# Optimization experiments

Hardware: AMD Instinct MI355X
Metric: run time of the kernel (lower is better)

Reference implementation:

```python
import jax, jax.numpy as jnp
import numpy as np

EMBED_DIM = 1024
NUM_HEADS = 16
HEAD_DIM = EMBED_DIM // NUM_HEADS
SEQ_LEN = 2048
BATCH = 2


def setup_inputs() -> dict:
    key = jax.random.key(0)
    ks = jax.random.split(key, 9)
    s = 1.0 / np.sqrt(EMBED_DIM)
    inputs = jax.random.normal(ks[0], (BATCH, SEQ_LEN, EMBED_DIM), dtype=jnp.float32)
    Wq = jax.random.uniform(ks[1], (EMBED_DIM, EMBED_DIM), jnp.float32, -s, s)
    bq = jax.random.uniform(ks[2], (EMBED_DIM,), jnp.float32, -s, s)
    Wk = jax.random.uniform(ks[3], (EMBED_DIM, EMBED_DIM), jnp.float32, -s, s)
    bk = jax.random.uniform(ks[4], (EMBED_DIM,), jnp.float32, -s, s)
    Wv = jax.random.uniform(ks[5], (EMBED_DIM, EMBED_DIM), jnp.float32, -s, s)
    bv = jax.random.uniform(ks[6], (EMBED_DIM,), jnp.float32, -s, s)
    Wo = jax.random.uniform(ks[7], (EMBED_DIM, EMBED_DIM), jnp.float32, -s, s)
    bo = jax.random.uniform(ks[8], (EMBED_DIM,), jnp.float32, -s, s)
    return {"inputs": inputs, "Wq": Wq, "bq": bq, "Wk": Wk, "bk": bk,
            "Wv": Wv, "bv": bv, "Wo": Wo, "bo": bo}


def reference(inputs, Wq, bq, Wk, bk, Wv, bv, Wo, bo):
    B, S, D = inputs.shape
    H, Hd = NUM_HEADS, HEAD_DIM

    def heads(x):  # [B,S,D] -> [B,H,S,Hd]
        return x.reshape(B, S, H, Hd).transpose(0, 2, 1, 3)

    q = heads(inputs @ Wq + bq)
    k = heads(inputs @ Wk + bk)
    v = heads(inputs @ Wv + bv)

    # [B,H,S,S] causal scores (naive, matching original module)
    scores = jnp.einsum('bhqd,bhkd->bhqk', q, k) * (Hd ** -0.5)
    causal = jnp.tril(jnp.ones((S, S), dtype=bool))
    scores = jnp.where(causal, scores, jnp.float32(-jnp.inf))
    attn = jax.nn.softmax(scores, axis=-1)

    out = jnp.einsum('bhqk,bhkd->bhqd', attn, v)
    out = out.transpose(0, 2, 1, 3).reshape(B, S, D)
    return out @ Wo + bo
```

## Files before the change

kernel.cpp:

```cpp
#include <hip/hip_runtime.h>
#include <stdint.h>
#include <stddef.h>

#define SEQ   2048
#define DIM   1024
#define NH    16
#define HD    64
#define MTOT  4096
#define LPAD  72
#define EPAD  136
#define FPAD  132

typedef __attribute__((ext_vector_type(8))) short short8;
typedef __attribute__((ext_vector_type(4))) float floatx4;
typedef __attribute__((ext_vector_type(16))) float floatx16;
typedef __attribute__((ext_vector_type(4))) float float4v;
typedef __attribute__((ext_vector_type(4))) unsigned short ushort4v;
typedef __attribute__((ext_vector_type(4))) unsigned int uint4v;

__device__ __forceinline__ floatx4 mfma_bf16(short8 a, short8 b, floatx4 c) {
    return __builtin_amdgcn_mfma_f32_16x16x32_bf16(a, b, c, 0, 0, 0);
}
__device__ __forceinline__ floatx16 mfma32(short8 a, short8 b, floatx16 c) {
    return __builtin_amdgcn_mfma_f32_32x32x16_bf16(a, b, c, 0, 0, 0);
}

__device__ __forceinline__ float b2f(unsigned short s) {
    unsigned int u = ((unsigned int)s) << 16;
    return __builtin_bit_cast(float, u);
}
__device__ __forceinline__ unsigned short f2b(float f) {
    unsigned int u = __builtin_bit_cast(unsigned int, f);
    u += 0x7fffu + ((u >> 16) & 1u);
    return (unsigned short)(u >> 16);
}
__device__ __forceinline__ unsigned int cvtpk(float lo, float hi) {
    unsigned int w;
    asm("v_cvt_pk_bf16_f32 %0, %1, %2" : "=v"(w) : "v"(lo), "v"(hi));
    return w;
}
__device__ __forceinline__ void swap32(unsigned int& a, unsigned int& b) {
    asm("v_permlane32_swap_b32 %0, %1" : "+v"(a), "+v"(b));
}
__device__ __forceinline__ short8 mk8(unsigned int a, unsigned int b,
                                      unsigned int c, unsigned int d) {
    uint4v u; u.x = a; u.y = b; u.z = c; u.w = d;
    return __builtin_bit_cast(short8, u);
}
__device__ __forceinline__ void g2l16(const unsigned short* g, unsigned short* l) {
    __builtin_amdgcn_global_load_lds(
        (const __attribute__((address_space(1))) void*)g,
        (__attribute__((address_space(3))) void*)l, 16, 0, 0);
}

__global__ __launch_bounds__(256) void cvt_f32_bf16(const float* __restrict__ in,
                                                    unsigned short* __restrict__ out) {
    const int i = (blockIdx.x * 256 + threadIdx.x) * 4;
    const float4v v = *(const float4v*)&in[i];
    ushort4v o;
    o.x = f2b(v.x); o.y = f2b(v.y); o.z = f2b(v.z); o.w = f2b(v.w);
    *(ushort4v*)&out[i] = o;
}

__global__ __launch_bounds__(256) void transpose_all(const float* __restrict__ w0,
                                                     const float* __restrict__ w1,
                                                     const float* __restrict__ w2,
                                                     const float* __restrict__ w3,
                                                     unsigned short* __restrict__ outbase) {
    __shared__ float t[64][65];
    const int z = blockIdx.z;
    const float* in = (z == 0) ? w0 : (z == 1) ? w1 : (z == 2) ? w2 : w3;
    unsigned short* out = outbase + (size_t)z * DIM * DIM;
    const int c0 = blockIdx.x * 64, r0 = blockIdx.y * 64;
    const int x = threadIdx.x, y = threadIdx.y;
#pragma unroll
    for (int i = 0; i < 64; i += 4)
        t[y + i][x] = in[(size_t)(r0 + y + i) * DIM + c0 + x];
    __syncthreads();
#pragma unroll
    for (int i = 0; i < 64; i += 4)
        out[(size_t)(c0 + y + i) * DIM + r0 + x] = f2b(t[x][y + i]);
}

__global__ __launch_bounds__(256) void gemm_fused(const unsigned short* __restrict__ A,
                                                  const unsigned short* __restrict__ WTbase,
                                                  const float* __restrict__ b0,
                                                  const float* __restrict__ b1,
                                                  const float* __restrict__ b2,
                                                  void* __restrict__ outbase,
                                                  int qkv) {
    __shared__ __attribute__((aligned(16))) unsigned short smem[2 * 128 * LPAD];
    unsigned short* As = smem;
    unsigned short* Bs = smem + 128 * 64;

    const int z = blockIdx.z;
    const unsigned short* BT = WTbase + (size_t)z * (DIM * DIM);
    const float* bias        = (z == 0) ? b0 : (z == 1) ? b1 : b2;
    const int mode = qkv ? ((z == 0) ? 1 : (z == 1) ? 3 : 4) : 0;
    float* Cf          = (float*)outbase;
    unsigned short* Cb = (unsigned short*)outbase + (size_t)z * ((size_t)MTOT * DIM);

    const int tid = threadIdx.x;
    const int w = tid >> 6, lane = tid & 63;
    const int quad = lane >> 4, l16 = lane & 15;
    const int wm = w >> 1, wn = w & 1;
    const int m0 = blockIdx.x * 128, n0 = blockIdx.y * 128;
    const int bb = m0 >> 11;

    floatx4 acc[4][4];
#pragma unroll
    for (int mi = 0; mi < 4; ++mi)
#pragma unroll
        for (int ni = 0; ni < 4; ++ni) acc[mi][ni] = (floatx4)0.0f;

    const int srow8 = lane >> 3;
    const int sgs8  = ((lane & 7) ^ srow8) * 8;
    const unsigned short* gA = &A [(size_t)(m0 + w * 8 + srow8) * DIM + sgs8];
    const unsigned short* gB = &BT[(size_t)(n0 + w * 8 + srow8) * DIM + sgs8];

    const int sx = l16 & 7;

    for (int k0 = 0; ; k0 += 64) {
#pragma unroll
        for (int i = 0; i < 4; ++i) {
            g2l16(gA + (size_t)i * (32 * DIM) + k0, &As[(i * 4 + w) * 512]);
            g2l16(gB + (size_t)i * (32 * DIM) + k0, &Bs[(i * 4 + w) * 512]);
        }
        __syncthreads();
#pragma unroll
        for (int kk = 0; kk < 2; ++kk) {
            short8 a[4], b[4];
#pragma unroll
            for (int mi = 0; mi < 4; ++mi)
                a[mi] = *(const short8*)&As[(wm * 64 + mi * 16 + l16) * 64 +
                                            (((kk * 4) + quad) ^ sx) * 8];
#pragma unroll
            for (int ni = 0; ni < 4; ++ni)
                b[ni] = *(const short8*)&Bs[(wn * 64 + ni * 16 + l16) * 64 +
                                            (((kk * 4) + quad) ^ sx) * 8];
#pragma unroll
            for (int mi = 0; mi < 4; ++mi)
#pragma unroll
                for (int ni = 0; ni < 4; ++ni)
                    acc[mi][ni] = mfma_bf16(a[mi], b[ni], acc[mi][ni]);
        }
        if (k0 + 64 >= DIM) break;
        __syncthreads();
    }

    float bvv[4];
#pragma unroll
    for (int ni = 0; ni < 4; ++ni) bvv[ni] = bias[n0 + wn * 64 + ni * 16 + l16];

    if (mode == 0) {
        float* T = (float*)smem;
        for (int p = 0; p < 4; ++p) {
            __syncthreads();
            if (wm == (p >> 1)) {
                const int mib = (p & 1) * 2;
#pragma unroll
                for (int mm = 0; mm < 2; ++mm)
#pragma unroll
                    for (int ni = 0; ni < 4; ++ni)
#pragma unroll
                        for (int r = 0; r < 4; ++r)
                            T[(mm * 16 + quad * 4 + r) * FPAD + wn * 64 + ni * 16 + l16] =
                                acc[mib + mm][ni][r] + bvv[ni];
            }
            __syncthreads();
#pragma unroll
            for (int it = 0; it < 4; ++it) {
                const int c = it * 256 + tid;
                const int row = c >> 5, nof = (c & 31) * 4;
                *(float4v*)&Cf[(size_t)(m0 + p * 32 + row) * DIM + n0 + nof] =
                    *(const float4v*)&T[row * FPAD + nof];
            }
        }
    } else if (mode == 1) {
        unsigned short* T = smem;
        __syncthreads();
#pragma unroll
        for (int mi = 0; mi < 4; ++mi)
#pragma unroll
            for (int ni = 0; ni < 4; ++ni)
#pragma unroll
                for (int r = 0; r < 4; ++r)
                    T[(wm * 64 + mi * 16 + quad * 4 + r) * EPAD + wn * 64 + ni * 16 + l16] =
                        f2b(acc[mi][ni][r] + bvv[ni]);
        __syncthreads();
#pragma unroll
        for (int it = 0; it < 8; ++it) {
            const int c = it * 256 + tid;
            const int seg = c >> 3, d8 = (c & 7) * 8;
            const int mm = seg >> 1, hseg = seg & 1;
            const int h = (n0 >> 6) + hseg;
            const int s = (m0 & (SEQ - 1)) + mm;
            *(short8*)&Cb[((size_t)(bb * NH + h) * SEQ + s) * HD + d8] =
                *(const short8*)&T[mm * EPAD + hseg * 64 + d8];
        }
    } else if (mode == 3) {
        unsigned short* T = smem;
        __syncthreads();
#pragma unroll
        for (int mi = 0; mi < 4; ++mi)
#pragma unroll
            for (int ni = 0; ni < 4; ++ni)
#pragma unroll
                for (int r = 0; r < 4; ++r)
                    T[(wm * 64 + mi * 16 + quad * 4 + r) * EPAD + wn * 64 + ni * 16 + l16] =
                        f2b(acc[mi][ni][r] + bvv[ni]);
        __syncthreads();
#pragma unroll
        for (int it = 0; it < 8; ++it) {
            const int f = it * 256 + tid;
            const int ln = f & 63, fragid = f >> 6;
            const int h2 = fragid >> 4;
            const int jb = (fragid >> 2) & 3;
            const int c  = fragid & 3;
            const short8 v = *(const short8*)&T[(jb * 32 + (ln & 31)) * EPAD +
                                                h2 * 64 + c * 16 + (ln >> 5) * 8];
            const int bh = bb * NH + (n0 >> 6) + h2;
            const int jg = ((m0 & (SEQ - 1)) >> 5) + jb;
            *(short8*)&Cb[(((size_t)bh * 64 + jg) * 4 + c) * 512 + ln * 8] = v;
        }
    } else {
        unsigned short* T = smem;
        __syncthreads();
#pragma unroll
        for (int mi = 0; mi < 4; ++mi)
#pragma unroll
            for (int ni = 0; ni < 4; ++ni) {
                ushort4v pk;
#pragma unroll
                for (int r = 0; r < 4; ++r) pk[r] = f2b(acc[mi][ni][r] + bvv[ni]);
                *(ushort4v*)&T[(wn * 64 + ni * 16 + l16) * EPAD + wm * 64 + mi * 16 + quad * 4] = pk;
            }
        __syncthreads();
#pragma unroll
        for (int it = 0; it < 8; ++it) {
            const int f = it * 256 + tid;
            const int ln = f & 63, fragid = f >> 6;
            const int h2 = fragid >> 4;
            const int jb = (fragid >> 2) & 3;
            const int dk = fragid & 3;
            const int d0 = dk >> 1, kk = dk & 1;
            const short8 v = *(const short8*)&T[(h2 * 64 + d0 * 32 + (ln & 31)) * EPAD +
                                                jb * 32 + kk * 16 + (ln >> 5) * 8];
            const int bh = bb * NH + (n0 >> 6) + h2;
            const int jg = ((m0 & (SEQ - 1)) >> 5) + jb;
            *(short8*)&Cb[(((size_t)bh * 64 + jg) * 4 + dk) * 512 + ln * 8] = v;
        }
    }
}

__global__ __launch_bounds__(64) void attn_fwd(const unsigned short* __restrict__ Q,
                                               const unsigned short* __restrict__ KP,
                                               const unsigned short* __restrict__ VP,
                                               unsigned short* __restrict__ O) {
    __shared__ __attribute__((aligned(16))) unsigned short Os[32 * LPAD];
    __shared__ float Linv[32];

    const int bh = blockIdx.x;
    const int qc = (gridDim.y - 1) - blockIdx.y;
    const int lane = threadIdx.x;
    const int ql  = lane & 31;
    const int hi  = lane >> 5;
    const int hi4 = hi * 4;
    const int hi8 = hi * 8;

    const unsigned short* Qh  = Q  + (size_t)bh * SEQ * HD;
    const unsigned short* KPh = KP + (size_t)bh * (64 * 2048);
    const unsigned short* VPh = VP + (size_t)bh * (64 * 2048);
    const int q0 = qc * 32;

    short8 qf[4];
#pragma unroll
    for (int c = 0; c < 4; ++c) {
        short8 t = *(const short8*)(Qh + (size_t)(q0 + ql) * HD + c * 16 + hi8);
        short8 o;
#pragma unroll
        for (int e = 0; e < 8; ++e)
            o[e] = (short)f2b(b2f((unsigned short)t[e]) * 0.125f);
        qf[c] = o;
    }

    floatx16 o_acc0 = (floatx16)0.0f, o_acc1 = (floatx16)0.0f;
    float l0 = 0.0f, l1 = 0.0f;

#define LOADKV(KF, VF, JJ) do {                                              \
        const unsigned short* kb_ = KPh + (size_t)(JJ) * 2048 + lane * 8;    \
        const unsigned short* vb_ = VPh + (size_t)(JJ) * 2048 + lane * 8;    \
        _Pragma("unroll")                                                    \
        for (int c_ = 0; c_ < 4; ++c_) {                                     \
            KF[c_] = *(const short8*)(kb_ + c_ * 512);                       \
            VF[c_] = *(const short8*)(vb_ + c_ * 512);                       \
        }                                                                    \
    } while (0)

#define ATT_BLOCK(KF, VF, MASKED) do {                                       \
        floatx16 st_ = (floatx16)0.0f;                                       \
        _Pragma("unroll")                                                    \
        for (int c_ = 0; c_ < 4; ++c_) st_ = mfma32(KF[c_], qf[c_], st_);    \
        float p_[16];                                                        \
        _Pragma("unroll")                                                    \
        for (int r_ = 0; r_ < 16; ++r_) {                                    \
            float e_ = __expf(st_[r_]);                                      \
            if (MASKED)                                                      \
                e_ = (((r_ & 3) + 8 * (r_ >> 2) + hi4) > ql) ? 0.0f : e_;    \
            p_[r_] = e_;                                                     \
        }                                                                    \
        l0 += (p_[0] + p_[1]) + (p_[2] + p_[3]);                             \
        l1 += (p_[4] + p_[5]) + (p_[6] + p_[7]);                             \
        l0 += (p_[8] + p_[9]) + (p_[10] + p_[11]);                           \
        l1 += (p_[12] + p_[13]) + (p_[14] + p_[15]);                         \
        unsigned int w0_ = cvtpk(p_[0], p_[1]),   w2_ = cvtpk(p_[4], p_[5]); \
        unsigned int w1_ = cvtpk(p_[2], p_[3]),   w3_ = cvtpk(p_[6], p_[7]); \
        unsigned int w4_ = cvtpk(p_[8], p_[9]),   w6_ = cvtpk(p_[12], p_[13]); \
        unsigned int w5_ = cvtpk(p_[10], p_[11]), w7_ = cvtpk(p_[14], p_[15]); \
        swap32(w0_, w2_); swap32(w1_, w3_);                                  \
        swap32(w4_, w6_); swap32(w5_, w7_);                                  \
        const short8 pa0_ = mk8(w0_, w1_, w2_, w3_);                         \
        const short8 pa1_ = mk8(w4_, w5_, w6_, w7_);                         \
        o_acc0 = mfma32(pa0_, VF[0], o_acc0);                                \
        o_acc0 = mfma32(pa1_, VF[1], o_acc0);                                \
        o_acc1 = mfma32(pa0_, VF[2], o_acc1);                                \
        o_acc1 = mfma32(pa1_, VF[3], o_acc1);                                \
    } while (0)

    short8 kfA[4], vfA[4], kfB[4], vfB[4];
    LOADKV(kfA, vfA, 0);
    int j = 0;
    while (j + 2 <= qc) {
        LOADKV(kfB, vfB, j + 1);
        ATT_BLOCK(kfA, vfA, 0);
        LOADKV(kfA, vfA, j + 2);
        ATT_BLOCK(kfB, vfB, 0);
        j += 2;
    }
    if (j < qc) {
        LOADKV(kfB, vfB, qc);
        ATT_BLOCK(kfA, vfA, 0);
        ATT_BLOCK(kfB, vfB, 1);
    } else {
        ATT_BLOCK(kfA, vfA, 1);
    }

    float l = l0 + l1;
    l += __shfl_xor(l, 32, 64);
    const float inv = 1.0f / l;
    if (lane < 32) Linv[lane] = inv;
    __syncthreads();
#pragma unroll
    for (int r = 0; r < 16; ++r) {
        const int row = (r & 3) + 8 * (r >> 2) + hi4;
        const float iv = Linv[row];
        Os[row * LPAD + ql]      = f2b(o_acc0[r] * iv);
        Os[row * LPAD + 32 + ql] = f2b(o_acc1[r] * iv);
    }
    __syncthreads();
    const int bb = bh >> 4, h = bh & 15;
#pragma unroll
    for (int it = 0; it < 4; ++it) {
        const int row = it * 8 + (lane >> 3), d8 = (lane & 7) * 8;
        *(short8*)&O[(size_t)(bb * SEQ + q0 + row) * DIM + h * HD + d8] =
            *(const short8*)&Os[row * LPAD + d8];
    }
#undef LOADKV
#undef ATT_BLOCK
}

extern "C" void kernel_launch(void* const* d_in, const int* in_sizes, int n_in,
                              void* d_out, int out_size, void* d_ws, size_t ws_size,
                              hipStream_t stream) {
    const float* X  = (const float*)d_in[0];
    const float* Wq = (const float*)d_in[1];
    const float* bq = (const float*)d_in[2];
    const float* Wk = (const float*)d_in[3];
    const float* bk = (const float*)d_in[4];
    const float* Wv = (const float*)d_in[5];
    const float* bv = (const float*)d_in[6];
    const float* Wo = (const float*)d_in[7];
    const float* bo = (const float*)d_in[8];

    unsigned short* ws = (unsigned short*)d_ws;
    const size_t WSZ = (size_t)DIM * DIM;
    const size_t TSZ = (size_t)MTOT * DIM;
    unsigned short* WqT = ws;
    unsigned short* WoT = ws + 3 * WSZ;
    unsigned short* Qb  = ws + 4 * WSZ;
    unsigned short* Kp  = Qb + TSZ;
    unsigned short* Vp  = Kp + TSZ;
    unsigned short* Ob  = Vp + TSZ;

    unsigned short* Xb = (unsigned short*)d_out;

    cvt_f32_bf16<<<dim3(TSZ / 1024), 256, 0, stream>>>(X, Xb);

    transpose_all<<<dim3(16, 16, 4), dim3(64, 4), 0, stream>>>(Wq, Wk, Wv, Wo, WqT);

    gemm_fused<<<dim3(MTOT / 128, DIM / 128, 3), 256, 0, stream>>>(
        Xb, WqT, bq, bk, bv, (void*)Qb, 1);

    attn_fwd<<<dim3(2 * NH, SEQ / 32), 64, 0, stream>>>(Qb, Kp, Vp, Ob);

    gemm_fused<<<dim3(MTOT / 128, DIM / 128, 1), 256, 0, stream>>>(
        Ob, WoT, bo, bo, bo, d_out, 0);
}
```

Before: 171.2 us.

## Split attention KV loop across four waves per block with LDS reduction

Each attention block now runs four waves, each handling every fourth KV block for the same 32 query rows. Their unnormalized outputs and row sums are combined through shared memory before normalizing and writing out. This cuts the serial KV chain per block, which is long for late query chunks, and adds MFMA priority hints. In exchange it uses more LDS and adds a cross-wave reduction, and waves on early query chunks sit idle.

```diff
diff --git a/kernel.cpp b/kernel.cpp
--- a/kernel.cpp
+++ b/kernel.cpp
@@ -253,16 +253,17 @@
     }
 }
 
-__global__ __launch_bounds__(64) void attn_fwd(const unsigned short* __restrict__ Q,
-                                               const unsigned short* __restrict__ KP,
-                                               const unsigned short* __restrict__ VP,
-                                               unsigned short* __restrict__ O) {
-    __shared__ __attribute__((aligned(16))) unsigned short Os[32 * LPAD];
-    __shared__ float Linv[32];
+__global__ __launch_bounds__(256) void attn_fwd(const unsigned short* __restrict__ Q,
+                                                const unsigned short* __restrict__ KP,
+                                                const unsigned short* __restrict__ VP,
+                                                unsigned short* __restrict__ O) {
+    __shared__ float Fo[4][32][68];
+    __shared__ float Fl[4][32];
 
     const int bh = blockIdx.x;
     const int qc = (gridDim.y - 1) - blockIdx.y;
-    const int lane = threadIdx.x;
+    const int tid = threadIdx.x;
+    const int w = tid >> 6, lane = tid & 63;
     const int ql  = lane & 31;
     const int hi  = lane >> 5;
     const int hi4 = hi * 4;
@@ -299,8 +300,10 @@
 
 #define ATT_BLOCK(KF, VF, MASKED) do {                                       \
         floatx16 st_ = (floatx16)0.0f;                                       \
+        __builtin_amdgcn_s_setprio(1);                                       \
         _Pragma("unroll")                                                    \
         for (int c_ = 0; c_ < 4; ++c_) st_ = mfma32(KF[c_], qf[c_], st_);    \
+        __builtin_amdgcn_s_setprio(0);                                       \
         float p_[16];                                                        \
         _Pragma("unroll")                                                    \
         for (int r_ = 0; r_ < 16; ++r_) {                                    \
@@ -321,50 +324,68 @@
         swap32(w4_, w6_); swap32(w5_, w7_);                                  \
         const short8 pa0_ = mk8(w0_, w1_, w2_, w3_);                         \
         const short8 pa1_ = mk8(w4_, w5_, w6_, w7_);                         \
+        __builtin_amdgcn_s_setprio(1);                                       \
         o_acc0 = mfma32(pa0_, VF[0], o_acc0);                                \
         o_acc0 = mfma32(pa1_, VF[1], o_acc0);                                \
         o_acc1 = mfma32(pa0_, VF[2], o_acc1);                                \
         o_acc1 = mfma32(pa1_, VF[3], o_acc1);                                \
+        __builtin_amdgcn_s_setprio(0);                                       \
     } while (0)
 
     short8 kfA[4], vfA[4], kfB[4], vfB[4];
-    LOADKV(kfA, vfA, 0);
-    int j = 0;
-    while (j + 2 <= qc) {
-        LOADKV(kfB, vfB, j + 1);
-        ATT_BLOCK(kfA, vfA, 0);
-        LOADKV(kfA, vfA, j + 2);
-        ATT_BLOCK(kfB, vfB, 0);
-        j += 2;
-    }
-    if (j < qc) {
-        LOADKV(kfB, vfB, qc);
-        ATT_BLOCK(kfA, vfA, 0);
-        ATT_BLOCK(kfB, vfB, 1);
-    } else {
-        ATT_BLOCK(kfA, vfA, 1);
-    }
-
+    int j = w;
+    if (j <= qc) {
+        LOADKV(kfA, vfA, j);
+        while (j + 8 <= qc) {
+            LOADKV(kfB, vfB, j + 4);
+            ATT_BLOCK(kfA, vfA, 0);
+            LOADKV(kfA, vfA, j + 8);
+            ATT_BLOCK(kfB, vfB, 0);
+            j += 8;
+        }
+        if (j + 4 <= qc) {
+            LOADKV(kfB, vfB, j + 4);
+            ATT_BLOCK(kfA, vfA, 0);
+            ATT_BLOCK(kfB, vfB, (j + 4) == qc);
+        } else {
+            ATT_BLOCK(kfA, vfA, j == qc);
+        }
+    }
+
+    float* Fow = &Fo[w][0][0];
+#pragma unroll
+    for (int r = 0; r < 16; ++r) {
+        const int row = (r & 3) + 8 * (r >> 2) + hi4;
+        Fow[row * 68 + ql]      = o_acc0[r];
+        Fow[row * 68 + 32 + ql] = o_acc1[r];
+    }
     float l = l0 + l1;
     l += __shfl_xor(l, 32, 64);
-    const float inv = 1.0f / l;
-    if (lane < 32) Linv[lane] = inv;
+    if (lane < 32) Fl[w][lane] = l;
     __syncthreads();
-#pragma unroll
-    for (int r = 0; r < 16; ++r) {
-        const int row = (r & 3) + 8 * (r >> 2) + hi4;
-        const float iv = Linv[row];
-        Os[row * LPAD + ql]      = f2b(o_acc0[r] * iv);
-        Os[row * LPAD + 32 + ql] = f2b(o_acc1[r] * iv);
-    }
-    __syncthreads();
+
+    const int rrow = w * 8 + (lane >> 3);
+    const int c8   = (lane & 7) * 8;
+    float s[8];
+#pragma unroll
+    for (int e = 0; e < 8; ++e) s[e] = 0.0f;
+#pragma unroll
+    for (int ww = 0; ww < 4; ++ww) {
+        const float* src = &Fo[ww][rrow][c8];
+        const float4v a = *(const float4v*)&src[0];
+        const float4v b = *(const float4v*)&src[4];
+        s[0] += a.x; s[1] += a.y; s[2] += a.z; s[3] += a.w;
+        s[4] += b.x; s[5] += b.y; s[6] += b.z; s[7] += b.w;
+    }
+    const float lt = (Fl[0][rrow] + Fl[1][rrow]) + (Fl[2][rrow] + Fl[3][rrow]);
+    const float iv = 1.0f / lt;
+    const unsigned int o0 = cvtpk(s[0] * iv, s[1] * iv);
+    const unsigned int o1 = cvtpk(s[2] * iv, s[3] * iv);
+    const unsigned int o2 = cvtpk(s[4] * iv, s[5] * iv);
+    const unsigned int o3 = cvtpk(s[6] * iv, s[7] * iv);
     const int bb = bh >> 4, h = bh & 15;
-#pragma unroll
-    for (int it = 0; it < 4; ++it) {
-        const int row = it * 8 + (lane >> 3), d8 = (lane & 7) * 8;
-        *(short8*)&O[(size_t)(bb * SEQ + q0 + row) * DIM + h * HD + d8] =
-            *(const short8*)&Os[row * LPAD + d8];
-    }
+    *(short8*)&O[(size_t)(bb * SEQ + q0 + rrow) * DIM + h * HD + c8] =
+        mk8(o0, o1, o2, o3);
 #undef LOADKV
 #undef ATT_BLOCK
 }
@@ -401,7 +422,7 @@
     gemm_fused<<<dim3(MTOT / 128, DIM / 128, 3), 256, 0, stream>>>(
         Xb, WqT, bq, bk, bv, (void*)Qb, 1);
 
-    attn_fwd<<<dim3(2 * NH, SEQ / 32), 64, 0, stream>>>(Qb, Kp, Vp, Ob);
+    attn_fwd<<<dim3(2 * NH, SEQ / 32), 256, 0, stream>>>(Qb, Kp, Vp, Ob);
 
     gemm_fused<<<dim3(MTOT / 128, DIM / 128, 1), 256, 0, stream>>>(
         Ob, WoT, bo, bo, bo, d_out, 0);
```

Result: no change. 169.9 us (-0.8%).
